# Optimization experiments

Hardware: AMD Instinct MI355X
Metric: run time of the kernel (lower is better)

The kernel has to match this reference:

```python
import jax, jax.numpy as jnp
import numpy as np

N_NODES = 50000
N_EDGES = 800000
NODE_DIM = 128
EDGE_DIM = 2
HID = 512
SLOPE = 0.15  # LeakyReLU negative slope


def _leaky(x):
    return jnp.where(x > 0, x, SLOPE * x)


def _lin(key, fan_in, fan_out, bias=True):
    s = 1.0 / np.sqrt(fan_in)
    k1, k2 = jax.random.split(key)
    W = jax.random.uniform(k1, (fan_in, fan_out), jnp.float32, -s, s)
    if not bias:
        return W
    b = jax.random.uniform(k2, (fan_out,), jnp.float32, -s, s)
    return W, b


def setup_inputs() -> dict:
    key = jax.random.key(0)
    ks = jax.random.split(key, 12)
    x = jax.random.normal(ks[0], (N_NODES, NODE_DIM), jnp.float32)
    edge_index = jax.random.randint(ks[1], (2, N_EDGES), 0, N_NODES, jnp.int32)
    edge_attr = jax.random.normal(ks[2], (N_EDGES, EDGE_DIM), jnp.float32)
    We, be = _lin(ks[3], EDGE_DIM, HID)
    # SAGEConv: out = lin_l(mean_agg(x_j)) + lin_r(x_i); lin_l has bias, lin_r does not
    W1l, b1 = _lin(ks[4], NODE_DIM, HID)
    W1r = _lin(ks[5], NODE_DIM, HID, bias=False)
    W2l, b2 = _lin(ks[6], HID, 256)
    W2r = _lin(ks[7], HID, 256, bias=False)
    W3l, b3 = _lin(ks[8], 256, 64)
    W3r = _lin(ks[9], 256, 64, bias=False)
    Wp, bp = _lin(ks[10], 64, 32)
    kf1, kf2 = jax.random.split(ks[11])
    Wf1, bf1 = _lin(kf1, 32, 32)
    Wf2, bf2 = _lin(kf2, 32, 2)
    return dict(x=x, edge_index=edge_index, edge_attr=edge_attr,
                We=We, be=be, W1l=W1l, b1=b1, W1r=W1r,
                W2l=W2l, b2=b2, W2r=W2r, W3l=W3l, b3=b3, W3r=W3r,
                Wp=Wp, bp=bp, Wf1=Wf1, bf1=bf1, Wf2=Wf2, bf2=bf2)


def _sage(h, src, dst, Wl, bl, Wr):
    # mean aggregation of source-node features at destination nodes
    n = h.shape[0]
    summed = jax.ops.segment_sum(h[src], dst, num_segments=n)          # [N, d]
    cnt = jax.ops.segment_sum(jnp.ones((src.shape[0],), h.dtype), dst, num_segments=n)
    mean = summed / jnp.maximum(cnt, 1.0)[:, None]
    return mean @ Wl + bl + h @ Wr


def reference(x, edge_index, edge_attr, We, be, W1l, b1, W1r,
              W2l, b2, W2r, W3l, b3, W3r, Wp, bp, Wf1, bf1, Wf2, bf2):
    src, dst = edge_index[0], edge_index[1]
    _edge_feats = edge_attr @ We + be  # computed in the original forward but never used downstream
    h = _leaky(_sage(x, src, dst, W1l, b1, W1r))   # dropout is identity in eval
    h = _leaky(_sage(h, src, dst, W2l, b2, W2r))
    h = _leaky(_sage(h, src, dst, W3l, b3, W3r))
    h = h @ Wp + bp                                 # pre_fc
    h = _leaky(h @ Wf1 + bf1)                       # classifier (Linear fallback)
    return h @ Wf2 + bf2                            # [N, 2]
```

## Files before the change

### kernel.cpp

```cpp
#include <hip/hip_runtime.h>
#include <hip/hip_fp16.h>

#define N_NODES 50000
#define N_EDGES 800000
#define SLOPE 0.15f

typedef unsigned short u16;
typedef __attribute__((ext_vector_type(8))) _Float16 f16x8;
typedef __attribute__((ext_vector_type(2))) _Float16 h16x2;
typedef __attribute__((ext_vector_type(4))) float f32x4;

static __device__ __forceinline__ float leaky(float v) { return v > 0.f ? v : SLOPE * v; }

static __device__ __forceinline__ u16 f2h(float v) {
    return __builtin_bit_cast(u16, __float2half(v));
}

static __device__ __forceinline__ float dot2acc(unsigned int u, float c) {
    h16x2 one = {(_Float16)1.0f, (_Float16)1.0f};
    return __builtin_amdgcn_fdot2(__builtin_bit_cast(h16x2, u), one, c, false);
}

static __device__ __forceinline__ void async_load16(const u16* g, u16* l) {
    __builtin_amdgcn_global_load_lds(
        (const __attribute__((address_space(1))) unsigned int*)g,
        (__attribute__((address_space(3))) unsigned int*)l, 16, 0, 0);
}

__global__ void k_prep(const int* __restrict__ dst, int* __restrict__ cnt,
                       int* __restrict__ erank,
                       const float* __restrict__ x, u16* __restrict__ xp,
                       const float* __restrict__ W1l, const float* __restrict__ W1r,
                       const float* __restrict__ W2l, const float* __restrict__ W2r,
                       const float* __restrict__ W3l, const float* __restrict__ W3r,
                       u16* w1lp, u16* w1rp, u16* w2cp, u16* w3cp) {
    int b = blockIdx.x, tid = threadIdx.x;
    if (b < 3125) {
        int e = b * 256 + tid;
        if (e < N_EDGES) erank[e] = atomicAdd(&cnt[dst[e]], 1);
        return;
    }
    b -= 3125;
    if (b < 6250) {
        int i = b * 256 + tid;
        if (i >= N_NODES * 32) return;
        float4 v = ((const float4*)x)[i];
        ((ushort4*)xp)[i] = make_ushort4(f2h(v.x), f2h(v.y), f2h(v.z), f2h(v.w));
        return;
    }
    b -= 6250;
    const float* W; u16* op; int K, N;
    if (b < 256)       { W = W1l; op = w1lp; K = 128; N = 512; }
    else if (b < 512)  { W = W1r; op = w1rp; K = 128; N = 512; b -= 256; }
    else if (b < 1024) { W = W2l; op = w2cp; K = 512; N = 256; b -= 512; }
    else if (b < 1536) { W = W2r; op = w2cp + 256 * 512; K = 512; N = 256; b -= 1024; }
    else if (b < 1600) { W = W3l; op = w3cp; K = 256; N = 64; b -= 1536; }
    else               { W = W3r; op = w3cp + 64 * 256; K = 256; N = 64; b -= 1600; }
    int i = b * 256 + tid;
    if (i >= K * N) return;
    int k = i / N, n = i - k * N;
    op[(size_t)n * K + k] = f2h(W[i]);
}

__global__ __launch_bounds__(1024) void k_scan1(const int* __restrict__ cnt,
                                                int* __restrict__ offs,
                                                int* __restrict__ bsum) {
    __shared__ int wsum[16];
    int tid = threadIdx.x, lane = tid & 63, wv = tid >> 6;
    int i = blockIdx.x * 1024 + tid;
    int c = (i < N_NODES) ? cnt[i] : 0;
    int orig = (c + 15) & ~15;
    int v = orig;
#pragma unroll
    for (int d = 1; d < 64; d <<= 1) {
        int t = __shfl_up(v, d, 64);
        if (lane >= d) v += t;
    }
    if (lane == 63) wsum[wv] = v;
    __syncthreads();
    if (wv == 0) {
        int s = (lane < 16) ? wsum[lane] : 0;
#pragma unroll
        for (int d = 1; d < 16; d <<= 1) {
            int t = __shfl_up(s, d, 64);
            if (lane >= d) s += t;
        }
        if (lane < 16) wsum[lane] = s;
        if (lane == 15) bsum[blockIdx.x] = s;
    }
    __syncthreads();
    int wpre = (wv == 0) ? 0 : wsum[wv - 1];
    if (i < N_NODES) offs[i] = v + wpre - orig;
}

__global__ void k_scan3(const int* __restrict__ cnt, int* __restrict__ offs,
                        float* __restrict__ inv, int* __restrict__ pssrc,
                        const int* __restrict__ bsum, int nb) {
    __shared__ int sb[64];
    int tid = threadIdx.x;
    if (tid < 64) {
        int v = (tid < nb) ? bsum[tid] : 0;
        int s = v;
#pragma unroll
        for (int d = 1; d < 64; d <<= 1) {
            int t = __shfl_up(s, d, 64);
            if (tid >= d) s += t;
        }
        sb[tid] = s - v;
        if (blockIdx.x == 0 && tid == nb - 1) offs[N_NODES] = s;
    }
    __syncthreads();
    int i = blockIdx.x * 256 + tid;
    if (i >= N_NODES) return;
    int c = cnt[i];
    int o = offs[i] + sb[i >> 10];
    offs[i] = o;
    inv[i] = 1.0f / (float)(c > 1 ? c : 1);
    int cp = (c + 15) & ~15;
    for (int j = c; j < cp; ++j) pssrc[o + j] = N_NODES;
}

__global__ void k_fill(const int* __restrict__ src, const int* __restrict__ dst,
                       const int* __restrict__ erank, const int* __restrict__ poffs,
                       int* __restrict__ pssrc) {
    int t = blockIdx.x * 256 + threadIdx.x;
    int e = t * 4;
    if (e + 3 >= N_EDGES) {
        for (; e < N_EDGES; ++e) pssrc[poffs[dst[e]] + erank[e]] = src[e];
        return;
    }
    int4 d4 = *(const int4*)&dst[e];
    int4 s4 = *(const int4*)&src[e];
    int4 r4 = *(const int4*)&erank[e];
    int p0 = poffs[d4.x] + r4.x;
    int p1 = poffs[d4.y] + r4.y;
    int p2 = poffs[d4.z] + r4.z;
    int p3 = poffs[d4.w] + r4.w;
    pssrc[p0] = s4.x;
    pssrc[p1] = s4.y;
    pssrc[p2] = s4.z;
    pssrc[p3] = s4.w;
}

template <int STRIDE, int EPI, int LPE, int U>
__global__ __launch_bounds__(256) void k_agg(const u16* __restrict__ tbl,
                                             const int* __restrict__ poffs,
                                             const int* __restrict__ pssrc,
                                             const float* __restrict__ inv,
                                             const u16* __restrict__ y,
                                             const float* __restrict__ bias,
                                             u16* __restrict__ outh,
                                             float* __restrict__ outf) {
    constexpr int G = 64 / LPE;
    int wid = (blockIdx.x * 256 + threadIdx.x) >> 6;
    if (wid >= N_NODES) return;
    int lane = threadIdx.x & 63;
    int g = lane / LPE;
    int cl = lane % LPE;
    int beg = poffs[wid], end = poffs[wid + 1];
    const u16* colbase = tbl + cl * 8;
    float acc[8] = {};
    for (int e = beg + g * U; e < end; e += G * U) {
        int idx[U];
        if constexpr (U == 4) {
            int4 t4 = *(const int4*)&pssrc[e];
            idx[0] = t4.x; idx[1] = t4.y; idx[2] = t4.z; idx[3] = t4.w;
        } else {
            int2 t2 = *(const int2*)&pssrc[e];
            idx[0] = t2.x; idx[1] = t2.y;
        }
        uint4 rv[U];
#pragma unroll
        for (int j = 0; j < U; ++j)
            rv[j] = *(const uint4*)(colbase + (size_t)idx[j] * STRIDE);
#pragma unroll
        for (int p = 0; p < U / 2; ++p) {
            const unsigned int* a = (const unsigned int*)&rv[2 * p];
            const unsigned int* b = (const unsigned int*)&rv[2 * p + 1];
#pragma unroll
            for (int t = 0; t < 4; ++t) {
                unsigned int lo = __builtin_amdgcn_perm(b[t], a[t], 0x05040100u);
                unsigned int hi = __builtin_amdgcn_perm(b[t], a[t], 0x07060302u);
                acc[2 * t + 0] = dot2acc(lo, acc[2 * t + 0]);
                acc[2 * t + 1] = dot2acc(hi, acc[2 * t + 1]);
            }
        }
    }
#pragma unroll
    for (int m = LPE; m < 64; m <<= 1)
#pragma unroll
        for (int t = 0; t < 8; ++t) acc[t] += __shfl_xor(acc[t], m, 64);
    if (g != 0) return;
    float wv = inv[wid];
    const size_t ob = (size_t)wid * STRIDE + cl * 8;
    float v[8];
    if constexpr (EPI == 0) {
#pragma unroll
        for (int t = 0; t < 8; ++t) v[t] = acc[t] * wv;
    } else {
        uint4 yv4 = *(const uint4*)(y + ob);
        const __half2* yp = (const __half2*)&yv4;
        float4 b0 = *(const float4*)(bias + cl * 8);
        float4 b1 = *(const float4*)(bias + cl * 8 + 4);
        float bb[8] = {b0.x, b0.y, b0.z, b0.w, b1.x, b1.y, b1.z, b1.w};
#pragma unroll
        for (int t = 0; t < 4; ++t) {
            float2 f = __half22float2(yp[t]);
            v[t * 2 + 0] = leaky(acc[t * 2 + 0] * wv + f.x + bb[t * 2 + 0]);
            v[t * 2 + 1] = leaky(acc[t * 2 + 1] * wv + f.y + bb[t * 2 + 1]);
        }
    }
    if constexpr (EPI == 3) {
        *(float4*)(outf + ob)     = make_float4(v[0], v[1], v[2], v[3]);
        *(float4*)(outf + ob + 4) = make_float4(v[4], v[5], v[6], v[7]);
    } else {
        *(ushort4*)(outh + ob)     = make_ushort4(f2h(v[0]), f2h(v[1]), f2h(v[2]), f2h(v[3]));
        *(ushort4*)(outh + ob + 4) = make_ushort4(f2h(v[4]), f2h(v[5]), f2h(v[6]), f2h(v[7]));
    }
}

__global__ __launch_bounds__(256, 5) void k_gemm_f(
    int M, int nct,
    const u16* __restrict__ A1, const u16* __restrict__ B1, int K1,
    const u16* __restrict__ A2, const u16* __restrict__ B2, int K2,
    const float* __restrict__ bias, int act, int colsplit,
    u16* __restrict__ out1h, int n1, u16* __restrict__ out2h, int n2) {
    __shared__ u16 Ash[2][4096], Bsh[2][4096];
    const int tid = threadIdx.x;
    const int lane = tid & 63;
    const int w = tid >> 6;
    const int wm = w & 1, wn = w >> 1;
    const int fr = lane & 15;
    const int q = lane >> 4;

    const int mT = (M + 127) >> 7;
    const int lin = blockIdx.x;
    const int grp = lin / (8 * nct);
    const int idx = lin - grp * (8 * nct);
    const int ct = idx >> 3;
    const int s8 = idx & 7;
    const int rowt = grp * 8 + s8;
    if (rowt >= mT) return;
    const int brow = rowt * 128;
    const int bcol = ct * 128;

    const int T1 = K1 >> 5, T = T1 + (K2 >> 5);

    const int c0 = (w * 2 + 0) * 64 + lane;
    const int c1 = (w * 2 + 1) * 64 + lane;
    const int r0 = c0 >> 2, g0 = (c0 & 3) ^ ((r0 >> 1) & 3);
    const int r1 = c1 >> 2, g1 = (c1 & 3) ^ ((r1 >> 1) & 3);
    int ar0 = brow + r0; if (ar0 >= M) ar0 = M - 1;
    int ar1 = brow + r1; if (ar1 >= M) ar1 = M - 1;
    const int br0 = bcol + r0, br1 = bcol + r1;
    const int ub0 = (w * 2 + 0) * 512;
    const int ub1 = (w * 2 + 1) * 512;

    auto stage = [&](int kt, int buf) {
        const u16 *A, *B; int K, k0;
        if (kt < T1) { A = A1; B = B1; K = K1; k0 = kt * 32; }
        else         { A = A2; B = B2; K = K2; k0 = (kt - T1) * 32; }
        async_load16(A + (size_t)ar0 * K + k0 + g0 * 8, &Ash[buf][ub0]);
        async_load16(A + (size_t)ar1 * K + k0 + g1 * 8, &Ash[buf][ub1]);
        async_load16(B + (size_t)br0 * K + k0 + g0 * 8, &Bsh[buf][ub0]);
        async_load16(B + (size_t)br1 * K + k0 + g1 * 8, &Bsh[buf][ub1]);
    };

    f32x4 acc[4][4] = {};

    stage(0, 0);
    __syncthreads();

    int cur = 0;
    for (int kt = 0; kt < T; ++kt) {
        if (kt + 1 < T) stage(kt + 1, cur ^ 1);
        f16x8 fa[4], fb[4];
#pragma unroll
        for (int rt = 0; rt < 4; ++rt) {
            int row = wm * 64 + rt * 16 + fr;
            int ad = row * 32 + ((q ^ ((row >> 1) & 3)) * 8);
            fa[rt] = __builtin_bit_cast(f16x8, *(const uint4*)&Ash[cur][ad]);
        }
#pragma unroll
        for (int ctf = 0; ctf < 4; ++ctf) {
            int row = wn * 64 + ctf * 16 + fr;
            int ad = row * 32 + ((q ^ ((row >> 1) & 3)) * 8);
            fb[ctf] = __builtin_bit_cast(f16x8, *(const uint4*)&Bsh[cur][ad]);
        }
#pragma unroll
        for (int rt = 0; rt < 4; ++rt)
#pragma unroll
            for (int ctf = 0; ctf < 4; ++ctf)
                acc[rt][ctf] = __builtin_amdgcn_mfma_f32_16x16x32_f16(fb[ctf], fa[rt], acc[rt][ctf], 0, 0, 0);
        if (kt + 1 < T) __syncthreads();
        cur ^= 1;
    }

#pragma unroll
    for (int rt = 0; rt < 4; ++rt) {
        int row = brow + wm * 64 + rt * 16 + fr;
        if (row >= M) continue;
#pragma unroll
        for (int ctf = 0; ctf < 4; ++ctf) {
            int col0 = bcol + wn * 64 + ctf * 16 + q * 4;
            float4 b4 = bias ? *(const float4*)(bias + col0) : make_float4(0.f, 0.f, 0.f, 0.f);
            float v0 = acc[rt][ctf][0] + b4.x;
            float v1 = acc[rt][ctf][1] + b4.y;
            float v2 = acc[rt][ctf][2] + b4.z;
            float v3 = acc[rt][ctf][3] + b4.w;
            if (act) { v0 = leaky(v0); v1 = leaky(v1); v2 = leaky(v2); v3 = leaky(v3); }
            ushort4 pk = make_ushort4(f2h(v0), f2h(v1), f2h(v2), f2h(v3));
            if (col0 < colsplit) *(ushort4*)(out1h + (size_t)row * n1 + col0) = pk;
            else                 *(ushort4*)(out2h + (size_t)row * n2 + (col0 - colsplit)) = pk;
        }
    }
}

__global__ __launch_bounds__(256, 6) void k_gemm_s(
    int M, int nct,
    const u16* __restrict__ A1, const u16* __restrict__ B1, int K1,
    const float* __restrict__ bias, int act, int colsplit,
    u16* __restrict__ out1h, int n1, u16* __restrict__ out2h, int n2) {
    __shared__ u16 Ash[2][4096], Bsh[2][2048];
    const int tid = threadIdx.x;
    const int lane = tid & 63;
    const int w = tid >> 6;
    const int wm = w & 1, wn = w >> 1;
    const int fr = lane & 15;
    const int q = lane >> 4;

    const int mT = (M + 127) >> 7;
    const int lin = blockIdx.x;
    const int grp = lin / (8 * nct);
    const int idx = lin - grp * (8 * nct);
    const int ct = idx >> 3;
    const int s8 = idx & 7;
    const int rowt = grp * 8 + s8;
    if (rowt >= mT) return;
    const int brow = rowt * 128;
    const int bcol = ct * 64;

    const int T = K1 >> 5;

    const int sA0 = (w * 2 + 0) * 64 + lane;
    const int sA1 = (w * 2 + 1) * 64 + lane;
    const int rA0 = sA0 >> 2, gA0 = (sA0 & 3) ^ ((rA0 >> 1) & 3);
    const int rA1 = sA1 >> 2, gA1 = (sA1 & 3) ^ ((rA1 >> 1) & 3);
    int ar0 = brow + rA0; if (ar0 >= M) ar0 = M - 1;
    int ar1 = brow + rA1; if (ar1 >= M) ar1 = M - 1;
    const int sB = w * 64 + lane;
    const int rB = sB >> 2, gB = (sB & 3) ^ ((rB >> 1) & 3);
    const int br = bcol + rB;
    const int ubA0 = (w * 2 + 0) * 512;
    const int ubA1 = (w * 2 + 1) * 512;
    const int ubB  = w * 512;

    auto stage = [&](int kt, int buf) {
        int k0 = kt * 32;
        async_load16(A1 + (size_t)ar0 * K1 + k0 + gA0 * 8, &Ash[buf][ubA0]);
        async_load16(A1 + (size_t)ar1 * K1 + k0 + gA1 * 8, &Ash[buf][ubA1]);
        async_load16(B1 + (size_t)br  * K1 + k0 + gB  * 8, &Bsh[buf][ubB]);
    };

    f32x4 acc[4][2] = {};

    stage(0, 0);
    __syncthreads();

    int cur = 0;
    for (int kt = 0; kt < T; ++kt) {
        if (kt + 1 < T) stage(kt + 1, cur ^ 1);
        f16x8 fa[4], fb[2];
#pragma unroll
        for (int rt = 0; rt < 4; ++rt) {
            int row = wm * 64 + rt * 16 + fr;
            int ad = row * 32 + ((q ^ ((row >> 1) & 3)) * 8);
            fa[rt] = __builtin_bit_cast(f16x8, *(const uint4*)&Ash[cur][ad]);
        }
#pragma unroll
        for (int ctf = 0; ctf < 2; ++ctf) {
            int row = wn * 32 + ctf * 16 + fr;
            int ad = row * 32 + ((q ^ ((row >> 1) & 3)) * 8);
            fb[ctf] = __builtin_bit_cast(f16x8, *(const uint4*)&Bsh[cur][ad]);
        }
#pragma unroll
        for (int rt = 0; rt < 4; ++rt)
#pragma unroll
            for (int ctf = 0; ctf < 2; ++ctf)
                acc[rt][ctf] = __builtin_amdgcn_mfma_f32_16x16x32_f16(fb[ctf], fa[rt], acc[rt][ctf], 0, 0, 0);
        if (kt + 1 < T) __syncthreads();
        cur ^= 1;
    }

#pragma unroll
    for (int rt = 0; rt < 4; ++rt) {
        int row = brow + wm * 64 + rt * 16 + fr;
        if (row >= M) continue;
#pragma unroll
        for (int ctf = 0; ctf < 2; ++ctf) {
            int col0 = bcol + wn * 32 + ctf * 16 + q * 4;
            float4 b4 = bias ? *(const float4*)(bias + col0) : make_float4(0.f, 0.f, 0.f, 0.f);
            float v0 = acc[rt][ctf][0] + b4.x;
            float v1 = acc[rt][ctf][1] + b4.y;
            float v2 = acc[rt][ctf][2] + b4.z;
            float v3 = acc[rt][ctf][3] + b4.w;
            if (act) { v0 = leaky(v0); v1 = leaky(v1); v2 = leaky(v2); v3 = leaky(v3); }
            ushort4 pk = make_ushort4(f2h(v0), f2h(v1), f2h(v2), f2h(v3));
            if (col0 < colsplit) *(ushort4*)(out1h + (size_t)row * n1 + col0) = pk;
            else                 *(ushort4*)(out2h + (size_t)row * n2 + (col0 - colsplit)) = pk;
        }
    }
}

__global__ __launch_bounds__(256) void k_head(const float* __restrict__ h3,
                                              const float* __restrict__ Wp, const float* __restrict__ bp,
                                              const float* __restrict__ Wf1, const float* __restrict__ bf1,
                                              const float* __restrict__ Wf2, const float* __restrict__ bf2,
                                              float* __restrict__ out) {
    __shared__ float sWp[64 * 32], sW1[32 * 32], sW2[32 * 2];
    __shared__ float sbp[32], sb1[32], sb2[2];
    int tid = threadIdx.x;
    for (int i = tid; i < 64 * 32; i += 256) sWp[i] = Wp[i];
    for (int i = tid; i < 32 * 32; i += 256) sW1[i] = Wf1[i];
    for (int i = tid; i < 64; i += 256) sW2[i] = Wf2[i];
    if (tid < 32) { sbp[tid] = bp[tid]; sb1[tid] = bf1[tid]; }
    if (tid < 2) sb2[tid] = bf2[tid];
    __syncthreads();
    int row = blockIdx.x * 256 + tid;
    if (row >= N_NODES) return;
    const float4* h4v = (const float4*)(h3 + (size_t)row * 64);
    float xr[64];
#pragma unroll
    for (int i = 0; i < 16; ++i) {
        float4 v = h4v[i];
        xr[i * 4 + 0] = v.x; xr[i * 4 + 1] = v.y;
        xr[i * 4 + 2] = v.z; xr[i * 4 + 3] = v.w;
    }
    float h4[32];
    for (int o = 0; o < 32; ++o) {
        float s = sbp[o];
#pragma unroll
        for (int i = 0; i < 64; ++i) s += xr[i] * sWp[i * 32 + o];
        h4[o] = s;
    }
    float h5[32];
    for (int o = 0; o < 32; ++o) {
        float s = sb1[o];
#pragma unroll
        for (int i = 0; i < 32; ++i) s += h4[i] * sW1[i * 32 + o];
        h5[o] = leaky(s);
    }
#pragma unroll
    for (int o = 0; o < 2; ++o) {
        float s = sb2[o];
#pragma unroll
        for (int i = 0; i < 32; ++i) s += h5[i] * sW2[i * 2 + o];
        out[(size_t)row * 2 + o] = s;
    }
}

extern "C" void kernel_launch(void* const* d_in, const int* in_sizes, int n_in,
                              void* d_out, int out_size, void* d_ws, size_t ws_size,
                              hipStream_t stream) {
    const float* x   = (const float*)d_in[0];
    const int*   ei  = (const int*)d_in[1];
    const float* W1l = (const float*)d_in[5];
    const float* b1  = (const float*)d_in[6];
    const float* W1r = (const float*)d_in[7];
    const float* W2l = (const float*)d_in[8];
    const float* b2  = (const float*)d_in[9];
    const float* W2r = (const float*)d_in[10];
    const float* W3l = (const float*)d_in[11];
    const float* b3  = (const float*)d_in[12];
    const float* W3r = (const float*)d_in[13];
    const float* Wp  = (const float*)d_in[14];
    const float* bp  = (const float*)d_in[15];
    const float* Wf1 = (const float*)d_in[16];
    const float* bf1 = (const float*)d_in[17];
    const float* Wf2 = (const float*)d_in[18];
    const float* bf2 = (const float*)d_in[19];
    float* out = (float*)d_out;
    (void)in_sizes; (void)n_in; (void)out_size; (void)ws_size;

    const int* src = ei;
    const int* dst = ei + N_EDGES;

    char* base = (char*)d_ws;
    size_t off = 0;
    auto alloc = [&](size_t bytes) -> void* {
        void* r = base + off;
        off = (off + bytes + 255) & ~(size_t)255;
        return r;
    };
    const size_t NN = N_NODES;
    int*   cnt    = (int*)alloc(NN * 4);
    int*   offs   = (int*)alloc((NN + 1) * 4);
    float* inv    = (float*)alloc(NN * 4);
    int*   bsum   = (int*)alloc(64 * 4);
    int*   erank  = (int*)alloc((size_t)N_EDGES * 4);
    int*   pssrc  = (int*)alloc((size_t)(N_EDGES + 16 * N_NODES) * 4);
    u16* w1lp = (u16*)alloc(128 * 512 * 2);
    u16* w1rp = (u16*)alloc(128 * 512 * 2);
    u16* w2cp = (u16*)alloc(512 * 512 * 2);
    u16* w3cp = (u16*)alloc(128 * 256 * 2);
    u16* xp  = (u16*)alloc((NN + 1) * 128 * 2);
    u16* axp = (u16*)alloc(NN * 128 * 2);
    u16* h1p = (u16*)alloc(NN * 512 * 2);
    u16* z2h = (u16*)alloc((NN + 1) * 256 * 2);
    u16* y2h = (u16*)alloc(NN * 256 * 2);
    u16* h2p = (u16*)alloc(NN * 256 * 2);
    u16* z3h = (u16*)alloc((NN + 1) * 64 * 2);
    u16* y3h = (u16*)alloc(NN * 64 * 2);
    float* h3f = (float*)alloc(NN * 64 * 4);

    hipMemsetAsync(cnt, 0, NN * 4, stream);
    hipMemsetAsync(xp + NN * 128, 0, 128 * 2, stream);
    hipMemsetAsync(z2h + NN * 256, 0, 256 * 2, stream);
    hipMemsetAsync(z3h + NN * 64, 0, 64 * 2, stream);
    k_prep<<<3125 + 6250 + 1664, 256, 0, stream>>>(dst, cnt, erank, x, xp,
        W1l, W1r, W2l, W2r, W3l, W3r, w1lp, w1rp, w2cp, w3cp);
    const int nb = (N_NODES + 1023) / 1024;
    k_scan1<<<nb, 1024, 0, stream>>>(cnt, offs, bsum);
    k_scan3<<<(N_NODES + 255) / 256, 256, 0, stream>>>(cnt, offs, inv, pssrc, bsum, nb);
    k_fill<<<(N_EDGES / 4 + 255) / 256, 256, 0, stream>>>(src, dst, erank, offs, pssrc);

    const int aggGrid = (N_NODES + 3) / 4;
    const int mT = (N_NODES + 127) / 128;
    const int grid4 = ((mT + 7) / 8) * 32;
    const int grid2s = ((mT + 7) / 8) * 8 * 2;

    k_agg<128, 0, 16, 4><<<aggGrid, 256, 0, stream>>>(
        xp, offs, pssrc, inv, nullptr, nullptr, axp, nullptr);
    k_gemm_f<<<grid4, 256, 0, stream>>>(N_NODES, 4,
        axp, w1lp, 128, xp, w1rp, 128, b1, 1, 512, h1p, 512, nullptr, 0);

    k_gemm_f<<<grid4, 256, 0, stream>>>(N_NODES, 4,
        h1p, w2cp, 512, nullptr, nullptr, 0, nullptr, 0, 256, z2h, 256, y2h, 256);
    k_agg<256, 2, 32, 4><<<aggGrid, 256, 0, stream>>>(
        z2h, offs, pssrc, inv, y2h, b2, h2p, nullptr);

    k_gemm_s<<<grid2s, 256, 0, stream>>>(N_NODES, 2,
        h2p, w3cp, 256, nullptr, 0, 64, z3h, 64, y3h, 64);
    k_agg<64, 3, 8, 2><<<aggGrid, 256, 0, stream>>>(
        z3h, offs, pssrc, inv, y3h, b3, nullptr, h3f);

    k_head<<<(N_NODES + 255) / 256, 256, 0, stream>>>(h3f,
        Wp, bp, Wf1, bf1, Wf2, bf2, out);
}
```

Before: 432.5 us.

## Fuse layer-3 aggregation with MLP head, widen GEMM tiles, fold memsets into prep

The last aggregation kernel and the separate head MLP kernel are merged, so the fp32 layer-3 activations are no longer written to and re-read from global memory. The head is computed cooperatively across the 8 lanes of each node using shuffles. The large GEMMs move from 128x128 to 128x256 tiles with more accumulators and launch bounds lowered to 2 blocks per CU, which improves A-tile reuse at the cost of occupancy and register pressure. The three small hipMemsetAsync calls for padding rows are folded into the prep kernel, removing three launches.

```diff
diff --git a/kernel.cpp b/kernel.cpp
--- a/kernel.cpp
+++ b/kernel.cpp
@@ -33,7 +33,8 @@
                        const float* __restrict__ W1l, const float* __restrict__ W1r,
                        const float* __restrict__ W2l, const float* __restrict__ W2r,
                        const float* __restrict__ W3l, const float* __restrict__ W3r,
-                       u16* w1lp, u16* w1rp, u16* w2cp, u16* w3cp) {
+                       u16* w1lp, u16* w1rp, u16* w2cp, u16* w3cp,
+                       u16* z2h, u16* z3h) {
     int b = blockIdx.x, tid = threadIdx.x;
     if (b < 3125) {
         int e = b * 256 + tid;
@@ -49,6 +50,13 @@
         return;
     }
     b -= 6250;
+    if (b >= 1664) {
+        int i = (b - 1664) * 256 + tid;
+        if (i < 128)      xp[(size_t)N_NODES * 128 + i] = 0;
+        else if (i < 384) z2h[(size_t)N_NODES * 256 + (i - 128)] = 0;
+        else if (i < 448) z3h[(size_t)N_NODES * 64 + (i - 384)] = 0;
+        return;
+    }
     const float* W; u16* op; int K, N;
     if (b < 256)       { W = W1l; op = w1lp; K = 128; N = 512; }
     else if (b < 512)  { W = W1r; op = w1rp; K = 128; N = 512; b -= 256; }
@@ -149,8 +157,7 @@
                                              const float* __restrict__ inv,
                                              const u16* __restrict__ y,
                                              const float* __restrict__ bias,
-                                             u16* __restrict__ outh,
-                                             float* __restrict__ outf) {
+                                             u16* __restrict__ outh) {
     constexpr int G = 64 / LPE;
     int wid = (blockIdx.x * 256 + threadIdx.x) >> 6;
     if (wid >= N_NODES) return;
@@ -210,22 +217,115 @@
             v[t * 2 + 1] = leaky(acc[t * 2 + 1] * wv + f.y + bb[t * 2 + 1]);
         }
     }
-    if constexpr (EPI == 3) {
-        *(float4*)(outf + ob)     = make_float4(v[0], v[1], v[2], v[3]);
-        *(float4*)(outf + ob + 4) = make_float4(v[4], v[5], v[6], v[7]);
-    } else {
-        *(ushort4*)(outh + ob)     = make_ushort4(f2h(v[0]), f2h(v[1]), f2h(v[2]), f2h(v[3]));
-        *(ushort4*)(outh + ob + 4) = make_ushort4(f2h(v[4]), f2h(v[5]), f2h(v[6]), f2h(v[7]));
-    }
-}
-
-__global__ __launch_bounds__(256, 5) void k_gemm_f(
-    int M, int nct,
+    *(ushort4*)(outh + ob)     = make_ushort4(f2h(v[0]), f2h(v[1]), f2h(v[2]), f2h(v[3]));
+    *(ushort4*)(outh + ob + 4) = make_ushort4(f2h(v[4]), f2h(v[5]), f2h(v[6]), f2h(v[7]));
+}
+
+__global__ __launch_bounds__(256) void k_agg_head(
+    const u16* __restrict__ tbl, const int* __restrict__ poffs,
+    const int* __restrict__ pssrc, const float* __restrict__ inv,
+    const u16* __restrict__ y, const float* __restrict__ bias,
+    const float* __restrict__ Wp, const float* __restrict__ bp,
+    const float* __restrict__ Wf1, const float* __restrict__ bf1,
+    const float* __restrict__ Wf2, const float* __restrict__ bf2,
+    float* __restrict__ out) {
+    constexpr int LPE = 8, U = 2, G = 8, STRIDE = 64;
+    __shared__ float sWp[64 * 32], sW1[32 * 32], sW2[64];
+    __shared__ float sbp[32], sb1[32], sb2[2];
+    int tid = threadIdx.x;
+    for (int i = tid; i < 64 * 32; i += 256) sWp[i] = Wp[i];
+    for (int i = tid; i < 32 * 32; i += 256) sW1[i] = Wf1[i];
+    if (tid < 64) sW2[tid] = Wf2[tid];
+    if (tid < 32) { sbp[tid] = bp[tid]; sb1[tid] = bf1[tid]; }
+    if (tid < 2) sb2[tid] = bf2[tid];
+    __syncthreads();
+    int wid = (blockIdx.x * 256 + tid) >> 6;
+    int lane = tid & 63;
+    int g = lane / LPE;
+    int cl = lane % LPE;
+    int beg = poffs[wid], end = poffs[wid + 1];
+    const u16* colbase = tbl + cl * 8;
+    float acc[8] = {};
+    for (int e = beg + g * U; e < end; e += G * U) {
+        int2 t2 = *(const int2*)&pssrc[e];
+        uint4 rv0 = *(const uint4*)(colbase + (size_t)t2.x * STRIDE);
+        uint4 rv1 = *(const uint4*)(colbase + (size_t)t2.y * STRIDE);
+        const unsigned int* a = (const unsigned int*)&rv0;
+        const unsigned int* b = (const unsigned int*)&rv1;
+#pragma unroll
+        for (int t = 0; t < 4; ++t) {
+            unsigned int lo = __builtin_amdgcn_perm(b[t], a[t], 0x05040100u);
+            unsigned int hi = __builtin_amdgcn_perm(b[t], a[t], 0x07060302u);
+            acc[2 * t + 0] = dot2acc(lo, acc[2 * t + 0]);
+            acc[2 * t + 1] = dot2acc(hi, acc[2 * t + 1]);
+        }
+    }
+#pragma unroll
+    for (int m = LPE; m < 64; m <<= 1)
+#pragma unroll
+        for (int t = 0; t < 8; ++t) acc[t] += __shfl_xor(acc[t], m, 64);
+    if (g != 0) return;
+    float wv = inv[wid];
+    const size_t ob = (size_t)wid * STRIDE + cl * 8;
+    uint4 yv4 = *(const uint4*)(y + ob);
+    const __half2* yp = (const __half2*)&yv4;
+    float4 b0 = *(const float4*)(bias + cl * 8);
+    float4 b1 = *(const float4*)(bias + cl * 8 + 4);
+    float bb[8] = {b0.x, b0.y, b0.z, b0.w, b1.x, b1.y, b1.z, b1.w};
+    float v[8];
+#pragma unroll
+    for (int t = 0; t < 4; ++t) {
+        float2 f = __half22float2(yp[t]);
+        v[t * 2 + 0] = leaky(acc[t * 2 + 0] * wv + f.x + bb[t * 2 + 0]);
+        v[t * 2 + 1] = leaky(acc[t * 2 + 1] * wv + f.y + bb[t * 2 + 1]);
+    }
+    float p[32];
+#pragma unroll
+    for (int o = 0; o < 32; ++o) p[o] = 0.f;
+#pragma unroll
+    for (int t = 0; t < 8; ++t) {
+        const float* wr = &sWp[(cl * 8 + t) * 32];
+        float vt = v[t];
+#pragma unroll
+        for (int o = 0; o < 32; ++o) p[o] += vt * wr[o];
+    }
+#pragma unroll
+    for (int m = 1; m < 8; m <<= 1)
+#pragma unroll
+        for (int o = 0; o < 32; ++o) p[o] += __shfl_xor(p[o], m, 64);
+#pragma unroll
+    for (int o = 0; o < 32; ++o) p[o] += sbp[o];
+    float h5[4];
+#pragma unroll
+    for (int oo = 0; oo < 4; ++oo) {
+        int o = cl * 4 + oo;
+        float s = sb1[o];
+#pragma unroll
+        for (int i = 0; i < 32; ++i) s += p[i] * sW1[i * 32 + o];
+        h5[oo] = leaky(s);
+    }
+    float o0 = 0.f, o1 = 0.f;
+#pragma unroll
+    for (int oo = 0; oo < 4; ++oo) {
+        int i = cl * 4 + oo;
+        o0 += h5[oo] * sW2[i * 2 + 0];
+        o1 += h5[oo] * sW2[i * 2 + 1];
+    }
+#pragma unroll
+    for (int m = 1; m < 8; m <<= 1) {
+        o0 += __shfl_xor(o0, m, 64);
+        o1 += __shfl_xor(o1, m, 64);
+    }
+    if (cl == 0) *(float2*)(out + (size_t)wid * 2) = make_float2(o0 + sb2[0], o1 + sb2[1]);
+}
+
+__global__ __launch_bounds__(256, 2) void k_gemm_w(
+    int M, int nct2,
     const u16* __restrict__ A1, const u16* __restrict__ B1, int K1,
     const u16* __restrict__ A2, const u16* __restrict__ B2, int K2,
     const float* __restrict__ bias, int act, int colsplit,
     u16* __restrict__ out1h, int n1, u16* __restrict__ out2h, int n2) {
-    __shared__ u16 Ash[2][4096], Bsh[2][4096];
+    __shared__ u16 Ash[2][4096], Bsh[2][8192];
     const int tid = threadIdx.x;
     const int lane = tid & 63;
     const int w = tid >> 6;
@@ -235,38 +335,46 @@
 
     const int mT = (M + 127) >> 7;
     const int lin = blockIdx.x;
-    const int grp = lin / (8 * nct);
-    const int idx = lin - grp * (8 * nct);
+    const int grp = lin / (8 * nct2);
+    const int idx = lin - grp * (8 * nct2);
     const int ct = idx >> 3;
     const int s8 = idx & 7;
     const int rowt = grp * 8 + s8;
     if (rowt >= mT) return;
     const int brow = rowt * 128;
-    const int bcol = ct * 128;
+    const int bcol = ct * 256;
 
     const int T1 = K1 >> 5, T = T1 + (K2 >> 5);
 
-    const int c0 = (w * 2 + 0) * 64 + lane;
-    const int c1 = (w * 2 + 1) * 64 + lane;
-    const int r0 = c0 >> 2, g0 = (c0 & 3) ^ ((r0 >> 1) & 3);
-    const int r1 = c1 >> 2, g1 = (c1 & 3) ^ ((r1 >> 1) & 3);
-    int ar0 = brow + r0; if (ar0 >= M) ar0 = M - 1;
-    int ar1 = brow + r1; if (ar1 >= M) ar1 = M - 1;
-    const int br0 = bcol + r0, br1 = bcol + r1;
-    const int ub0 = (w * 2 + 0) * 512;
-    const int ub1 = (w * 2 + 1) * 512;
+    const int cA0 = (w * 2 + 0) * 64 + lane;
+    const int cA1 = (w * 2 + 1) * 64 + lane;
+    const int rA0 = cA0 >> 2, gA0 = (cA0 & 3) ^ ((rA0 >> 1) & 3);
+    const int rA1 = cA1 >> 2, gA1 = (cA1 & 3) ^ ((rA1 >> 1) & 3);
+    int ar0 = brow + rA0; if (ar0 >= M) ar0 = M - 1;
+    int ar1 = brow + rA1; if (ar1 >= M) ar1 = M - 1;
+    int rB[4], gB[4];
+#pragma unroll
+    for (int j = 0; j < 4; ++j) {
+        int s = (w * 4 + j) * 64 + lane;
+        rB[j] = s >> 2;
+        gB[j] = (s & 3) ^ ((rB[j] >> 1) & 3);
+    }
+    const int ubA0 = (w * 2 + 0) * 512;
+    const int ubA1 = (w * 2 + 1) * 512;
 
     auto stage = [&](int kt, int buf) {
         const u16 *A, *B; int K, k0;
         if (kt < T1) { A = A1; B = B1; K = K1; k0 = kt * 32; }
         else         { A = A2; B = B2; K = K2; k0 = (kt - T1) * 32; }
-        async_load16(A + (size_t)ar0 * K + k0 + g0 * 8, &Ash[buf][ub0]);
-        async_load16(A + (size_t)ar1 * K + k0 + g1 * 8, &Ash[buf][ub1]);
-        async_load16(B + (size_t)br0 * K + k0 + g0 * 8, &Bsh[buf][ub0]);
-        async_load16(B + (size_t)br1 * K + k0 + g1 * 8, &Bsh[buf][ub1]);
+        async_load16(A + (size_t)ar0 * K + k0 + gA0 * 8, &Ash[buf][ubA0]);
+        async_load16(A + (size_t)ar1 * K + k0 + gA1 * 8, &Ash[buf][ubA1]);
+#pragma unroll
+        for (int j = 0; j < 4; ++j)
+            async_load16(B + (size_t)(bcol + rB[j]) * K + k0 + gB[j] * 8,
+                         &Bsh[buf][(w * 4 + j) * 512]);
     };
 
-    f32x4 acc[4][4] = {};
+    f32x4 acc[4][8] = {};
 
     stage(0, 0);
     __syncthreads();
@@ -274,7 +382,7 @@
     int cur = 0;
     for (int kt = 0; kt < T; ++kt) {
         if (kt + 1 < T) stage(kt + 1, cur ^ 1);
-        f16x8 fa[4], fb[4];
+        f16x8 fa[4], fb[8];
 #pragma unroll
         for (int rt = 0; rt < 4; ++rt) {
             int row = wm * 64 + rt * 16 + fr;
@@ -282,16 +390,16 @@
             fa[rt] = __builtin_bit_cast(f16x8, *(const uint4*)&Ash[cur][ad]);
         }
 #pragma unroll
-        for (int ctf = 0; ctf < 4; ++ctf) {
-            int row = wn * 64 + ctf * 16 + fr;
+        for (int cf = 0; cf < 8; ++cf) {
+            int row = wn * 128 + cf * 16 + fr;
             int ad = row * 32 + ((q ^ ((row >> 1) & 3)) * 8);
-            fb[ctf] = __builtin_bit_cast(f16x8, *(const uint4*)&Bsh[cur][ad]);
+            fb[cf] = __builtin_bit_cast(f16x8, *(const uint4*)&Bsh[cur][ad]);
         }
 #pragma unroll
         for (int rt = 0; rt < 4; ++rt)
 #pragma unroll
-            for (int ctf = 0; ctf < 4; ++ctf)
-                acc[rt][ctf] = __builtin_amdgcn_mfma_f32_16x16x32_f16(fb[ctf], fa[rt], acc[rt][ctf], 0, 0, 0);
+            for (int cf = 0; cf < 8; ++cf)
+                acc[rt][cf] = __builtin_amdgcn_mfma_f32_16x16x32_f16(fb[cf], fa[rt], acc[rt][cf], 0, 0, 0);
         if (kt + 1 < T) __syncthreads();
         cur ^= 1;
     }
@@ -301,13 +409,13 @@
         int row = brow + wm * 64 + rt * 16 + fr;
         if (row >= M) continue;
 #pragma unroll
-        for (int ctf = 0; ctf < 4; ++ctf) {
-            int col0 = bcol + wn * 64 + ctf * 16 + q * 4;
+        for (int cf = 0; cf < 8; ++cf) {
+            int col0 = bcol + wn * 128 + cf * 16 + q * 4;
             float4 b4 = bias ? *(const float4*)(bias + col0) : make_float4(0.f, 0.f, 0.f, 0.f);
-            float v0 = acc[rt][ctf][0] + b4.x;
-            float v1 = acc[rt][ctf][1] + b4.y;
-            float v2 = acc[rt][ctf][2] + b4.z;
-            float v3 = acc[rt][ctf][3] + b4.w;
+            float v0 = acc[rt][cf][0] + b4.x;
+            float v1 = acc[rt][cf][1] + b4.y;
+            float v2 = acc[rt][cf][2] + b4.z;
+            float v3 = acc[rt][cf][3] + b4.w;
             if (act) { v0 = leaky(v0); v1 = leaky(v1); v2 = leaky(v2); v3 = leaky(v3); }
             ushort4 pk = make_ushort4(f2h(v0), f2h(v1), f2h(v2), f2h(v3));
             if (col0 < colsplit) *(ushort4*)(out1h + (size_t)row * n1 + col0) = pk;
@@ -409,53 +517,6 @@
             if (col0 < colsplit) *(ushort4*)(out1h + (size_t)row * n1 + col0) = pk;
             else                 *(ushort4*)(out2h + (size_t)row * n2 + (col0 - colsplit)) = pk;
         }
-    }
-}
-
-__global__ __launch_bounds__(256) void k_head(const float* __restrict__ h3,
-                                              const float* __restrict__ Wp, const float* __restrict__ bp,
-                                              const float* __restrict__ Wf1, const float* __restrict__ bf1,
-                                              const float* __restrict__ Wf2, const float* __restrict__ bf2,
-                                              float* __restrict__ out) {
-    __shared__ float sWp[64 * 32], sW1[32 * 32], sW2[32 * 2];
-    __shared__ float sbp[32], sb1[32], sb2[2];
-    int tid = threadIdx.x;
-    for (int i = tid; i < 64 * 32; i += 256) sWp[i] = Wp[i];
-    for (int i = tid; i < 32 * 32; i += 256) sW1[i] = Wf1[i];
-    for (int i = tid; i < 64; i += 256) sW2[i] = Wf2[i];
-    if (tid < 32) { sbp[tid] = bp[tid]; sb1[tid] = bf1[tid]; }
-    if (tid < 2) sb2[tid] = bf2[tid];
-    __syncthreads();
-    int row = blockIdx.x * 256 + tid;
-    if (row >= N_NODES) return;
-    const float4* h4v = (const float4*)(h3 + (size_t)row * 64);
-    float xr[64];
-#pragma unroll
-    for (int i = 0; i < 16; ++i) {
-        float4 v = h4v[i];
-        xr[i * 4 + 0] = v.x; xr[i * 4 + 1] = v.y;
-        xr[i * 4 + 2] = v.z; xr[i * 4 + 3] = v.w;
-    }
-    float h4[32];
-    for (int o = 0; o < 32; ++o) {
-        float s = sbp[o];
-#pragma unroll
-        for (int i = 0; i < 64; ++i) s += xr[i] * sWp[i * 32 + o];
-        h4[o] = s;
-    }
-    float h5[32];
-    for (int o = 0; o < 32; ++o) {
-        float s = sb1[o];
-#pragma unroll
-        for (int i = 0; i < 32; ++i) s += h4[i] * sW1[i * 32 + o];
-        h5[o] = leaky(s);
-    }
-#pragma unroll
-    for (int o = 0; o < 2; ++o) {
-        float s = sb2[o];
-#pragma unroll
-        for (int i = 0; i < 32; ++i) s += h5[i] * sW2[i * 2 + o];
-        out[(size_t)row * 2 + o] = s;
     }
 }
 
@@ -511,39 +572,32 @@
     u16* h2p = (u16*)alloc(NN * 256 * 2);
     u16* z3h = (u16*)alloc((NN + 1) * 64 * 2);
     u16* y3h = (u16*)alloc(NN * 64 * 2);
-    float* h3f = (float*)alloc(NN * 64 * 4);
 
     hipMemsetAsync(cnt, 0, NN * 4, stream);
-    hipMemsetAsync(xp + NN * 128, 0, 128 * 2, stream);
-    hipMemsetAsync(z2h + NN * 256, 0, 256 * 2, stream);
-    hipMemsetAsync(z3h + NN * 64, 0, 64 * 2, stream);
-    k_prep<<<3125 + 6250 + 1664, 256, 0, stream>>>(dst, cnt, erank, x, xp,
-        W1l, W1r, W2l, W2r, W3l, W3r, w1lp, w1rp, w2cp, w3cp);
+    k_prep<<<3125 + 6250 + 1664 + 2, 256, 0, stream>>>(dst, cnt, erank, x, xp,
+        W1l, W1r, W2l, W2r, W3l, W3r, w1lp, w1rp, w2cp, w3cp, z2h, z3h);
     const int nb = (N_NODES + 1023) / 1024;
     k_scan1<<<nb, 1024, 0, stream>>>(cnt, offs, bsum);
     k_scan3<<<(N_NODES + 255) / 256, 256, 0, stream>>>(cnt, offs, inv, pssrc, bsum, nb);
     k_fill<<<(N_EDGES / 4 + 255) / 256, 256, 0, stream>>>(src, dst, erank, offs, pssrc);
 
-    const int aggGrid = (N_NODES + 3) / 4;
+    const int aggGrid = N_NODES / 4;
     const int mT = (N_NODES + 127) / 128;
-    const int grid4 = ((mT + 7) / 8) * 32;
+    const int gridW = ((mT + 7) / 8) * 8 * 2;
     const int grid2s = ((mT + 7) / 8) * 8 * 2;
 
     k_agg<128, 0, 16, 4><<<aggGrid, 256, 0, stream>>>(
-        xp, offs, pssrc, inv, nullptr, nullptr, axp, nullptr);
-    k_gemm_f<<<grid4, 256, 0, stream>>>(N_NODES, 4,
+        xp, offs, pssrc, inv, nullptr, nullptr, axp);
+    k_gemm_w<<<gridW, 256, 0, stream>>>(N_NODES, 2,
         axp, w1lp, 128, xp, w1rp, 128, b1, 1, 512, h1p, 512, nullptr, 0);
 
-    k_gemm_f<<<grid4, 256, 0, stream>>>(N_NODES, 4,
+    k_gemm_w<<<gridW, 256, 0, stream>>>(N_NODES, 2,
         h1p, w2cp, 512, nullptr, nullptr, 0, nullptr, 0, 256, z2h, 256, y2h, 256);
     k_agg<256, 2, 32, 4><<<aggGrid, 256, 0, stream>>>(
-        z2h, offs, pssrc, inv, y2h, b2, h2p, nullptr);
+        z2h, offs, pssrc, inv, y2h, b2, h2p);
 
     k_gemm_s<<<grid2s, 256, 0, stream>>>(N_NODES, 2,
         h2p, w3cp, 256, nullptr, 0, 64, z3h, 64, y3h, 64);
-    k_agg<64, 3, 8, 2><<<aggGrid, 256, 0, stream>>>(
-        z3h, offs, pssrc, inv, y3h, b3, nullptr, h3f);
-
-    k_head<<<(N_NODES + 255) / 256, 256, 0, stream>>>(h3f,
-        Wp, bp, Wf1, bf1, Wf2, bf2, out);
-}
+    k_agg_head<<<aggGrid, 256, 0, stream>>>(
+        z3h, offs, pssrc, inv, y3h, b3, Wp, bp, Wf1, bf1, Wf2, bf2, out);
+}
```

Result: slower. 532.3 us (+23.1%).
